# Performance work log

Hardware: AMD Instinct MI355X
Metric: run time of the kernel (lower is better)

The kernel has to match this reference:

```python
import jax, jax.numpy as jnp
import numpy as np

B, N, E, H = 16, 1024, 1024, 16
D = E // H  # head size = 64

def setup_inputs() -> dict:
    key = jax.random.key(0)
    ks = jax.random.split(key, 5)
    s = 1.0 / np.sqrt(E)
    return {
        "x": jax.random.normal(ks[0], (B, N, E), dtype=jnp.float32),
        "W_qkv": jax.random.normal(ks[1], (E, 3 * E), dtype=jnp.float32) * s,
        "b_qkv": jnp.zeros((3 * E,), dtype=jnp.float32),
        "W_proj": jax.random.normal(ks[2], (E, E), dtype=jnp.float32) * s,
        "b_proj": jnp.zeros((E,), dtype=jnp.float32),
    }

def reference(x, W_qkv, b_qkv, W_proj, b_proj):
    # qkv projection: [B,N,3E]
    qkv = x @ W_qkv + b_qkv
    q, k, v = jnp.split(qkv, 3, axis=-1)
    # b n (h d) -> b h n d
    def split_heads(t):
        return t.reshape(B, N, H, D).transpose(0, 2, 1, 3)
    q, k, v = split_heads(q), split_heads(k), split_heads(v)
    scale = D ** -0.5
    attn = jnp.einsum('bhnd,bhmd->bhnm', q, k) * scale  # [B,H,N,N]
    attn = jax.nn.softmax(attn, axis=-1)
    # dropout p=0 -> identity
    o = jnp.einsum('bhnm,bhmd->bhnd', attn, v)  # [B,H,N,D]
    o = o.transpose(0, 2, 1, 3).reshape(B, N, E)  # b h n d -> b n (h d)
    return o @ W_proj + b_proj
```

## Files before the change

kernel.cpp:

```cpp
#include <hip/hip_runtime.h>
#include <hip/hip_bf16.h>
#include <math.h>

#define BB 16
#define NN 1024
#define EE 1024
#define HH 16
#define DD 64
#define THREE_E 3072
#define M_TOTAL (BB * NN)

typedef __attribute__((ext_vector_type(8))) short bf16x8;
typedef __attribute__((ext_vector_type(4))) short bf16x4;
typedef __attribute__((ext_vector_type(4))) float floatx4;

#define SCALE_Q 0.18033688011112042f

static __device__ __forceinline__ unsigned short f2bf(float f) {
    union { float f; unsigned u; } x; x.f = f;
    unsigned r = x.u + 0x7fffu + ((x.u >> 16) & 1u);
    return (unsigned short)(r >> 16);
}

static __device__ __forceinline__ float fast_exp2(float x) {
#if __has_builtin(__builtin_amdgcn_exp2f)
    return __builtin_amdgcn_exp2f(x);
#else
    float r; __asm__("v_exp_f32 %0, %1" : "=v"(r) : "v"(x)); return r;
#endif
}

static __device__ __forceinline__ bf16x8 pack8v(floatx4 a, floatx4 b) {
    union { bf16x8 v; unsigned u[4]; } r;
    __hip_bfloat162 t;
    t = __float22bfloat162_rn(make_float2(a[0], a[1])); r.u[0] = *(unsigned*)&t;
    t = __float22bfloat162_rn(make_float2(a[2], a[3])); r.u[1] = *(unsigned*)&t;
    t = __float22bfloat162_rn(make_float2(b[0], b[1])); r.u[2] = *(unsigned*)&t;
    t = __float22bfloat162_rn(make_float2(b[2], b[3])); r.u[3] = *(unsigned*)&t;
    return r.v;
}
static __device__ __forceinline__ bf16x8 pack8f(float4 a, float4 b) {
    union { bf16x8 v; unsigned u[4]; } r;
    __hip_bfloat162 t;
    t = __float22bfloat162_rn(make_float2(a.x, a.y)); r.u[0] = *(unsigned*)&t;
    t = __float22bfloat162_rn(make_float2(a.z, a.w)); r.u[1] = *(unsigned*)&t;
    t = __float22bfloat162_rn(make_float2(b.x, b.y)); r.u[2] = *(unsigned*)&t;
    t = __float22bfloat162_rn(make_float2(b.z, b.w)); r.u[3] = *(unsigned*)&t;
    return r.v;
}

#define ASYNC16(gp, lp)                                                \
    __builtin_amdgcn_global_load_lds(                                  \
        (const __attribute__((address_space(1))) void*)(gp),           \
        (__attribute__((address_space(3))) void*)(lp), 16, 0, 0)

#define DRAIN_VMEM() __asm__ __volatile__("s_waitcnt vmcnt(0)" ::: "memory")

__global__ __launch_bounds__(256) void prep_all(
    const float* __restrict__ x, unsigned short* __restrict__ xb,
    const float* __restrict__ Wqkv, unsigned short* __restrict__ Wqt,
    const float* __restrict__ Wproj, unsigned short* __restrict__ Wpt)
{
    __shared__ float tile[32][33];
    const int bid = blockIdx.x;
    const int t = threadIdx.x;

    if (bid < 8192) {
        int i = bid * 256 + t;
        const float4* xp = (const float4*)x;
        float4 a = xp[i * 2], b = xp[i * 2 + 1];
        *(bf16x8*)&xb[i * 8] = pack8f(a, b);
        return;
    }

    const float* w; unsigned short* wt; int R, C, bx, by;
    if (bid < 8192 + 3072) {
        int local = bid - 8192;
        bx = local % 96; by = local / 96;
        w = Wqkv; wt = Wqt; R = EE; C = THREE_E;
    } else {
        int local = bid - 11264;
        bx = local % 32; by = local / 32;
        w = Wproj; wt = Wpt; R = EE; C = EE;
    }
    const int lr = t >> 5, lc = t & 31;
    const int r0 = by * 32, c0 = bx * 32;
    #pragma unroll
    for (int p = 0; p < 4; ++p)
        tile[lr + p * 8][lc] = w[(size_t)(r0 + lr + p * 8) * C + c0 + lc];
    __syncthreads();
    #pragma unroll
    for (int p = 0; p < 4; ++p) {
        int oc = lr + p * 8;
        float v = tile[lc][oc];
        wt[(size_t)(c0 + oc) * R + r0 + lc] = f2bf(v);
    }
}

__global__ __launch_bounds__(256, 2) void gemm_qkv_mfma(
    const unsigned short* __restrict__ xb,
    const unsigned short* __restrict__ wt,
    const float* __restrict__ bias,
    unsigned short* __restrict__ Qo, unsigned short* __restrict__ Ko,
    unsigned short* __restrict__ Vo)
{
    __shared__ __align__(16) unsigned short As[256 * 64];
    __shared__ __align__(16) unsigned short Bs[128 * 64];

    const int t = threadIdx.x;
    const int w = t >> 6, lane = t & 63;
    const int quad = lane >> 4, l15 = lane & 15;
    const int wm = w >> 1, wn = w & 1;
    const int m0 = blockIdx.y * 256;
    const int n0 = blockIdx.x * 128;
    const int srow = lane >> 3;
    const int sch  = lane & 7;
    const int scw  = (sch ^ srow) * 8;
    const int rb   = l15 & 7;

    floatx4 acc[8][4];
    #pragma unroll
    for (int i = 0; i < 8; ++i)
        #pragma unroll
        for (int j = 0; j < 4; ++j) acc[i][j] = (floatx4){0.f, 0.f, 0.f, 0.f};

    const unsigned short* aG = &xb[(size_t)(m0 + w * 8 + srow) * EE + scw];
    const unsigned short* bG = &wt[(size_t)(n0 + w * 8 + srow) * EE + scw];

    for (int kk = 0; kk < EE; kk += 64) {
        #pragma unroll
        for (int p = 0; p < 8; ++p)
            ASYNC16(aG + kk + (size_t)(p * 32) * EE, &As[(w * 8 + p * 32) * 64]);
        #pragma unroll
        for (int p = 0; p < 4; ++p)
            ASYNC16(bG + kk + (size_t)(p * 32) * EE, &Bs[(w * 8 + p * 32) * 64]);
        DRAIN_VMEM();
        __syncthreads();

        #pragma unroll
        for (int s = 0; s < 2; ++s) {
            const int rsw = (((s << 2) | quad) ^ rb) * 8;
            bf16x8 af[8], bf[4];
            #pragma unroll
            for (int j = 0; j < 4; ++j)
                bf[j] = *(const bf16x8*)&Bs[(wn * 64 + j * 16 + l15) * 64 + rsw];
            #pragma unroll
            for (int i = 0; i < 8; ++i)
                af[i] = *(const bf16x8*)&As[(wm * 128 + i * 16 + l15) * 64 + rsw];
            __builtin_amdgcn_s_setprio(1);
            #pragma unroll
            for (int i = 0; i < 8; ++i)
                #pragma unroll
                for (int j = 0; j < 4; ++j)
                    acc[i][j] = __builtin_amdgcn_mfma_f32_16x16x32_bf16(
                        af[i], bf[j], acc[i][j], 0, 0, 0);
            __builtin_amdgcn_s_setprio(0);
        }
        __syncthreads();
    }

    const int mb = m0 + wm * 128;
    const int nb = n0 + wn * 64;
    #pragma unroll
    for (int i = 0; i < 8; ++i) {
        #pragma unroll
        for (int j = 0; j < 4; ++j) {
            int nc = nb + j * 16;
            int which = nc >> 10;
            int e0 = nc & 1023;
            int h  = e0 >> 6;
            int d0 = e0 & 63;
            float bv = bias[nc + l15];
            #pragma unroll
            for (int r = 0; r < 4; ++r) {
                int m = mb + i * 16 + quad * 4 + r;
                int b = m >> 10, n = m & 1023;
                size_t off = ((size_t)(b * HH + h) * NN + n) * DD + d0 + l15;
                float v = acc[i][j][r] + bv;
                if (which == 0)      Qo[off] = f2bf(v * SCALE_Q);
                else if (which == 1) Ko[off] = f2bf(v);
                else                 Vo[off] = f2bf(v);
            }
        }
    }
}

__global__ __launch_bounds__(256) void attn_mfma(
    const unsigned short* __restrict__ Q,
    const unsigned short* __restrict__ K,
    const unsigned short* __restrict__ Vn,
    unsigned short* __restrict__ O)
{
    __shared__ __align__(16) unsigned short Ks[2][64 * 64];
    __shared__ __align__(16) unsigned short Vs[2][64 * 64];

    const int t    = threadIdx.x;
    const int w    = t >> 6;
    const int quad = (t >> 4) & 3;
    const int l15  = t & 15;
    const int i    = blockIdx.x;
    const int bh   = ((i >> 6) << 3) | (i & 7);
    const int qt   = (i >> 3) & 7;

    const unsigned short* Qg = Q  + (size_t)bh * NN * DD;
    const unsigned short* Kg = K  + (size_t)bh * NN * DD;
    const unsigned short* Vg = Vn + (size_t)bh * NN * DD;

    const int q0 = qt * 128 + w * 32;

    bf16x8 qf[2][2];
    #pragma unroll
    for (int a = 0; a < 2; ++a) {
        qf[a][0] = *(const bf16x8*)&Qg[(size_t)(q0 + a * 16 + l15) * DD + quad * 8];
        qf[a][1] = *(const bf16x8*)&Qg[(size_t)(q0 + a * 16 + l15) * DD + 32 + quad * 8];
    }

    bf16x8 onesA;
    #pragma unroll
    for (int z = 0; z < 8; ++z) onesA[z] = (short)0x3F80;

    floatx4 oa[2][4];
    #pragma unroll
    for (int a = 0; a < 2; ++a)
        #pragma unroll
        for (int jd = 0; jd < 4; ++jd) oa[a][jd] = (floatx4){0.f, 0.f, 0.f, 0.f};
    floatx4 ls[2];
    ls[0] = (floatx4){0.f, 0.f, 0.f, 0.f};
    ls[1] = (floatx4){0.f, 0.f, 0.f, 0.f};

    const int srow = t >> 2;
    const int sc   = t & 3;
    const int swz  = srow & 7;
    const int cbase = ((quad ^ (l15 & 7)) << 3);

    const int Bk = ((srow >> 2) & 3) | (((srow >> 5) & 1) << 2);
    const int c0 = (((srow >> 4) & 1) << 2) | (srow & 3);

    bf16x8 krA0, krA1, vrA0, vrA1;
    bf16x8 krB0, krB1, vrB0, vrB1;

#define LOADKV(T, k0, k1, v0, v1) do {                                      \
    const unsigned short* kg_ = &Kg[(size_t)((T) * 64 + srow) * DD + sc * 16];\
    k0 = *(const bf16x8*)&kg_[0];                                           \
    k1 = *(const bf16x8*)&kg_[8];                                           \
    const unsigned short* vg_ = &Vg[(size_t)((T) * 64 + srow) * DD + sc * 16];\
    v0 = *(const bf16x8*)&vg_[0];                                           \
    v1 = *(const bf16x8*)&vg_[8]; } while (0)

#define WRITEKV(S, k0, k1, v0, v1) do {                                     \
    *(bf16x8*)&Ks[S][srow * 64 + (((2 * sc + 0) ^ swz) << 3)] = k0;         \
    *(bf16x8*)&Ks[S][srow * 64 + (((2 * sc + 1) ^ swz) << 3)] = k1;         \
    _Pragma("unroll")                                                       \
    for (int z = 0; z < 8; ++z) {                                           \
        const int swb = ((Bk ^ z) << 3) + c0;                               \
        const int dB = (sc * 16 + z) * 64;                                  \
        Vs[S][dB + swb]       = v0[z];                                      \
        Vs[S][dB + 512 + swb] = v1[z];                                      \
    } } while (0)

#define COMPUTE(S) do {                                                     \
    floatx4 sa[2][4];                                                       \
    _Pragma("unroll")                                                       \
    for (int a = 0; a < 2; ++a)                                             \
        _Pragma("unroll")                                                   \
        for (int tt = 0; tt < 4; ++tt) sa[a][tt] = (floatx4){0.f,0.f,0.f,0.f};\
    __builtin_amdgcn_s_setprio(1);                                          \
    _Pragma("unroll")                                                       \
    for (int tt = 0; tt < 4; ++tt) {                                        \
        const unsigned short* kb = &Ks[S][(tt * 16 + l15) * 64];            \
        bf16x8 kf0 = *(const bf16x8*)&kb[cbase];                            \
        bf16x8 kf1 = *(const bf16x8*)&kb[cbase ^ 32];                       \
        _Pragma("unroll")                                                   \
        for (int a = 0; a < 2; ++a) {                                       \
            sa[a][tt] = __builtin_amdgcn_mfma_f32_16x16x32_bf16(            \
                kf0, qf[a][0], sa[a][tt], 0, 0, 0);                         \
            sa[a][tt] = __builtin_amdgcn_mfma_f32_16x16x32_bf16(            \
                kf1, qf[a][1], sa[a][tt], 0, 0, 0);                         \
        }                                                                   \
    }                                                                       \
    __builtin_amdgcn_s_setprio(0);                                          \
    bf16x8 pf[2][2];                                                        \
    _Pragma("unroll")                                                       \
    for (int a = 0; a < 2; ++a) {                                           \
        floatx4 pe[4];                                                      \
        _Pragma("unroll")                                                   \
        for (int tt = 0; tt < 4; ++tt) {                                    \
            _Pragma("unroll")                                               \
            for (int r = 0; r < 4; ++r)                                     \
                pe[tt][r] = fast_exp2(sa[a][tt][r]);                        \
        }                                                                   \
        pf[a][0] = pack8v(pe[0], pe[1]);                                    \
        pf[a][1] = pack8v(pe[2], pe[3]);                                    \
    }                                                                       \
    __builtin_amdgcn_s_setprio(1);                                          \
    _Pragma("unroll")                                                       \
    for (int a = 0; a < 2; ++a) {                                           \
        ls[a] = __builtin_amdgcn_mfma_f32_16x16x32_bf16(                    \
            onesA, pf[a][0], ls[a], 0, 0, 0);                               \
        ls[a] = __builtin_amdgcn_mfma_f32_16x16x32_bf16(                    \
            onesA, pf[a][1], ls[a], 0, 0, 0);                               \
    }                                                                       \
    _Pragma("unroll")                                                       \
    for (int jd = 0; jd < 4; ++jd) {                                        \
        const unsigned short* vb = &Vs[S][(jd * 16 + l15) * 64];            \
        bf16x8 vf0 = *(const bf16x8*)&vb[cbase];                            \
        bf16x8 vf1 = *(const bf16x8*)&vb[cbase ^ 32];                       \
        _Pragma("unroll")                                                   \
        for (int a = 0; a < 2; ++a) {                                       \
            oa[a][jd] = __builtin_amdgcn_mfma_f32_16x16x32_bf16(            \
                vf0, pf[a][0], oa[a][jd], 0, 0, 0);                         \
            oa[a][jd] = __builtin_amdgcn_mfma_f32_16x16x32_bf16(            \
                vf1, pf[a][1], oa[a][jd], 0, 0, 0);                         \
        }                                                                   \
    }                                                                       \
    __builtin_amdgcn_s_setprio(0); } while (0)

    LOADKV(0, krA0, krA1, vrA0, vrA1);
    WRITEKV(0, krA0, krA1, vrA0, vrA1);
    LOADKV(1, krB0, krB1, vrB0, vrB1);
    __syncthreads();

    #pragma unroll 1
    for (int p = 0; p < 8; ++p) {
        WRITEKV(1, krB0, krB1, vrB0, vrB1);
        if (p < 7) LOADKV(2 * p + 2, krA0, krA1, vrA0, vrA1);
        COMPUTE(0);
        __syncthreads();
        if (p < 7) {
            WRITEKV(0, krA0, krA1, vrA0, vrA1);
            LOADKV(2 * p + 3, krB0, krB1, vrB0, vrB1);
        }
        COMPUTE(1);
        __syncthreads();
    }
#undef LOADKV
#undef WRITEKV
#undef COMPUTE

    const int b = bh >> 4, h = bh & 15;
    #pragma unroll
    for (int a = 0; a < 2; ++a) {
        float inv = 1.f / ls[a][0];
        int n = q0 + a * 16 + l15;
        size_t base = (size_t)(b * NN + n) * EE + h * DD;
        #pragma unroll
        for (int jd = 0; jd < 4; ++jd) {
            bf16x4 v;
            v[0] = (short)f2bf(oa[a][jd][0] * inv);
            v[1] = (short)f2bf(oa[a][jd][1] * inv);
            v[2] = (short)f2bf(oa[a][jd][2] * inv);
            v[3] = (short)f2bf(oa[a][jd][3] * inv);
            *(bf16x4*)&O[base + jd * 16 + quad * 4] = v;
        }
    }
}

__global__ __launch_bounds__(256, 2) void gemm_proj_mfma(
    const unsigned short* __restrict__ Ob,
    const unsigned short* __restrict__ Bp,
    const float* __restrict__ bias, float* __restrict__ out)
{
    __shared__ __align__(16) unsigned short As[256 * 64];
    __shared__ __align__(16) unsigned short Bs[128 * 64];

    const int t = threadIdx.x;
    const int w = t >> 6, lane = t & 63;
    const int quad = lane >> 4, l15 = lane & 15;
    const int wm = w >> 1, wn = w & 1;
    const int m0 = blockIdx.y * 256;
    const int n0 = blockIdx.x * 128;
    const int srow = lane >> 3;
    const int sch  = lane & 7;
    const int scw  = (sch ^ srow) * 8;
    const int rb   = l15 & 7;

    floatx4 acc[8][4];
    #pragma unroll
    for (int i = 0; i < 8; ++i)
        #pragma unroll
        for (int j = 0; j < 4; ++j) acc[i][j] = (floatx4){0.f, 0.f, 0.f, 0.f};

    const unsigned short* aG = &Ob[(size_t)(m0 + w * 8 + srow) * EE + scw];
    const unsigned short* bG = &Bp[(size_t)(n0 + w * 8 + srow) * EE + scw];

    for (int kk = 0; kk < EE; kk += 64) {
        #pragma unroll
        for (int p = 0; p < 8; ++p)
            ASYNC16(aG + kk + (size_t)(p * 32) * EE, &As[(w * 8 + p * 32) * 64]);
        #pragma unroll
        for (int p = 0; p < 4; ++p)
            ASYNC16(bG + kk + (size_t)(p * 32) * EE, &Bs[(w * 8 + p * 32) * 64]);
        DRAIN_VMEM();
        __syncthreads();

        #pragma unroll
        for (int s = 0; s < 2; ++s) {
            const int rsw = (((s << 2) | quad) ^ rb) * 8;
            bf16x8 af[8], bf[4];
            #pragma unroll
            for (int j = 0; j < 4; ++j)
                bf[j] = *(const bf16x8*)&Bs[(wn * 64 + j * 16 + l15) * 64 + rsw];
            #pragma unroll
            for (int i = 0; i < 8; ++i)
                af[i] = *(const bf16x8*)&As[(wm * 128 + i * 16 + l15) * 64 + rsw];
            __builtin_amdgcn_s_setprio(1);
            #pragma unroll
            for (int i = 0; i < 8; ++i)
                #pragma unroll
                for (int j = 0; j < 4; ++j)
                    acc[i][j] = __builtin_amdgcn_mfma_f32_16x16x32_bf16(
                        af[i], bf[j], acc[i][j], 0, 0, 0);
            __builtin_amdgcn_s_setprio(0);
        }
        __syncthreads();
    }

    const int mb = m0 + wm * 128;
    const int nb = n0 + wn * 64;
    #pragma unroll
    for (int i = 0; i < 8; ++i) {
        #pragma unroll
        for (int j = 0; j < 4; ++j) {
            float bv = bias[nb + j * 16 + l15];
            #pragma unroll
            for (int r = 0; r < 4; ++r) {
                int mrow = mb + i * 16 + quad * 4 + r;
                out[(size_t)mrow * EE + nb + j * 16 + l15] = acc[i][j][r] + bv;
            }
        }
    }
}

extern "C" void kernel_launch(void* const* d_in, const int* in_sizes, int n_in,
                              void* d_out, int out_size, void* d_ws, size_t ws_size,
                              hipStream_t stream) {
    const float* x     = (const float*)d_in[0];
    const float* Wqkv  = (const float*)d_in[1];
    const float* bqkv  = (const float*)d_in[2];
    const float* Wproj = (const float*)d_in[3];
    const float* bproj = (const float*)d_in[4];
    float* out = (float*)d_out;

    const size_t BHND = (size_t)BB * HH * NN * DD;
    unsigned short* Q   = (unsigned short*)d_ws;
    unsigned short* K   = Q   + BHND;
    unsigned short* Vn  = K   + BHND;
    unsigned short* Ob  = Vn  + BHND;
    unsigned short* xb  = Ob  + BHND;
    unsigned short* Wqt = xb  + BHND;
    unsigned short* Wpt = Wqt + (size_t)THREE_E * EE;

    dim3 blk(256);
    prep_all<<<dim3(12288), blk, 0, stream>>>(x, xb, Wqkv, Wqt, Wproj, Wpt);

    gemm_qkv_mfma<<<dim3(THREE_E / 128, M_TOTAL / 256), blk, 0, stream>>>(
        xb, Wqt, bqkv, Q, K, Vn);
    attn_mfma<<<dim3(BB * HH * NN / 128), blk, 0, stream>>>(Q, K, Vn, Ob);
    gemm_proj_mfma<<<dim3(EE / 128, M_TOTAL / 256), blk, 0, stream>>>(
        Ob, Wpt, bproj, out);
}
```

Before: 374.8 us.

## Double-buffer LDS tiles with async prefetch in QKV and projection GEMMs

Both GEMM kernels switch from a single 64-wide K tile, loaded and then fully drained each iteration, to two 32-wide K buffers. The next chunk is prefetched with global_load_lds while the current one is consumed, and a partial vmcnt wait replaces the full drain. The LDS footprint stays the same, but the XOR swizzle changes to fit the 4-chunk row width. In exchange, the K loop runs twice as many iterations with two barriers each.

Result: slower. 393.1 us (+4.9%).

```diff
diff --git a/kernel.cpp b/kernel.cpp
--- a/kernel.cpp
+++ b/kernel.cpp
@@ -53,8 +53,6 @@
     __builtin_amdgcn_global_load_lds(                                  \
         (const __attribute__((address_space(1))) void*)(gp),           \
         (__attribute__((address_space(3))) void*)(lp), 16, 0, 0)
-
-#define DRAIN_VMEM() __asm__ __volatile__("s_waitcnt vmcnt(0)" ::: "memory")
 
 __global__ __launch_bounds__(256) void prep_all(
     const float* __restrict__ x, unsigned short* __restrict__ xb,
@@ -104,8 +102,8 @@
     unsigned short* __restrict__ Qo, unsigned short* __restrict__ Ko,
     unsigned short* __restrict__ Vo)
 {
-    __shared__ __align__(16) unsigned short As[256 * 64];
-    __shared__ __align__(16) unsigned short Bs[128 * 64];
+    __shared__ __align__(16) unsigned short As[2][256 * 32];
+    __shared__ __align__(16) unsigned short Bs[2][128 * 32];
 
     const int t = threadIdx.x;
     const int w = t >> 6, lane = t & 63;
@@ -113,10 +111,10 @@
     const int wm = w >> 1, wn = w & 1;
     const int m0 = blockIdx.y * 256;
     const int n0 = blockIdx.x * 128;
-    const int srow = lane >> 3;
-    const int sch  = lane & 7;
-    const int scw  = (sch ^ srow) * 8;
-    const int rb   = l15 & 7;
+    const int srow = lane >> 2;
+    const int sch  = lane & 3;
+    const int scw  = (sch ^ ((srow ^ (srow >> 2)) & 3)) * 8;
+    const int rsw  = ((quad ^ ((l15 ^ (l15 >> 2)) & 3))) * 8;
 
     floatx4 acc[8][4];
     #pragma unroll
@@ -124,40 +122,51 @@
         #pragma unroll
         for (int j = 0; j < 4; ++j) acc[i][j] = (floatx4){0.f, 0.f, 0.f, 0.f};
 
-    const unsigned short* aG = &xb[(size_t)(m0 + w * 8 + srow) * EE + scw];
-    const unsigned short* bG = &wt[(size_t)(n0 + w * 8 + srow) * EE + scw];
-
-    for (int kk = 0; kk < EE; kk += 64) {
-        #pragma unroll
-        for (int p = 0; p < 8; ++p)
-            ASYNC16(aG + kk + (size_t)(p * 32) * EE, &As[(w * 8 + p * 32) * 64]);
-        #pragma unroll
-        for (int p = 0; p < 4; ++p)
-            ASYNC16(bG + kk + (size_t)(p * 32) * EE, &Bs[(w * 8 + p * 32) * 64]);
-        DRAIN_VMEM();
-        __syncthreads();
-
-        #pragma unroll
-        for (int s = 0; s < 2; ++s) {
-            const int rsw = (((s << 2) | quad) ^ rb) * 8;
-            bf16x8 af[8], bf[4];
+    const unsigned short* aG = &xb[(size_t)(m0 + w * 16 + srow) * EE + scw];
+    const unsigned short* bG = &wt[(size_t)(n0 + w * 16 + srow) * EE + scw];
+
+#define STG(c, sl) do {                                                     \
+    _Pragma("unroll")                                                       \
+    for (int p = 0; p < 4; ++p)                                             \
+        ASYNC16(aG + (c) * 32 + (size_t)(p * 64) * EE,                      \
+                &As[sl][(w * 16 + p * 64) * 32]);                           \
+    _Pragma("unroll")                                                       \
+    for (int p = 0; p < 2; ++p)                                             \
+        ASYNC16(bG + (c) * 32 + (size_t)(p * 64) * EE,                      \
+                &Bs[sl][(w * 16 + p * 64) * 32]);                           \
+    } while (0)
+
+    STG(0, 0);
+
+    #pragma unroll 1
+    for (int c = 0; c < 32; ++c) {
+        const int cur = c & 1;
+        if (c + 1 < 32) {
+            STG(c + 1, cur ^ 1);
+            __asm__ __volatile__("s_waitcnt vmcnt(6)" ::: "memory");
+        } else {
+            __asm__ __volatile__("s_waitcnt vmcnt(0)" ::: "memory");
+        }
+        __builtin_amdgcn_s_barrier();
+
+        bf16x8 af[8], bfv[4];
+        #pragma unroll
+        for (int j = 0; j < 4; ++j)
+            bfv[j] = *(const bf16x8*)&Bs[cur][(wn * 64 + j * 16 + l15) * 32 + rsw];
+        #pragma unroll
+        for (int i = 0; i < 8; ++i)
+            af[i] = *(const bf16x8*)&As[cur][(wm * 128 + i * 16 + l15) * 32 + rsw];
+        __builtin_amdgcn_s_setprio(1);
+        #pragma unroll
+        for (int i = 0; i < 8; ++i)
             #pragma unroll
             for (int j = 0; j < 4; ++j)
-                bf[j] = *(const bf16x8*)&Bs[(wn * 64 + j * 16 + l15) * 64 + rsw];
-            #pragma unroll
-            for (int i = 0; i < 8; ++i)
-                af[i] = *(const bf16x8*)&As[(wm * 128 + i * 16 + l15) * 64 + rsw];
-            __builtin_amdgcn_s_setprio(1);
-            #pragma unroll
-            for (int i = 0; i < 8; ++i)
-                #pragma unroll
-                for (int j = 0; j < 4; ++j)
-                    acc[i][j] = __builtin_amdgcn_mfma_f32_16x16x32_bf16(
-                        af[i], bf[j], acc[i][j], 0, 0, 0);
-            __builtin_amdgcn_s_setprio(0);
-        }
-        __syncthreads();
-    }
+                acc[i][j] = __builtin_amdgcn_mfma_f32_16x16x32_bf16(
+                    af[i], bfv[j], acc[i][j], 0, 0, 0);
+        __builtin_amdgcn_s_setprio(0);
+        __builtin_amdgcn_s_barrier();
+    }
+#undef STG
 
     const int mb = m0 + wm * 128;
     const int nb = n0 + wn * 64;
@@ -360,8 +369,8 @@
     const unsigned short* __restrict__ Bp,
     const float* __restrict__ bias, float* __restrict__ out)
 {
-    __shared__ __align__(16) unsigned short As[256 * 64];
-    __shared__ __align__(16) unsigned short Bs[128 * 64];
+    __shared__ __align__(16) unsigned short As[2][256 * 32];
+    __shared__ __align__(16) unsigned short Bs[2][128 * 32];
 
     const int t = threadIdx.x;
     const int w = t >> 6, lane = t & 63;
@@ -369,10 +378,10 @@
     const int wm = w >> 1, wn = w & 1;
     const int m0 = blockIdx.y * 256;
     const int n0 = blockIdx.x * 128;
-    const int srow = lane >> 3;
-    const int sch  = lane & 7;
-    const int scw  = (sch ^ srow) * 8;
-    const int rb   = l15 & 7;
+    const int srow = lane >> 2;
+    const int sch  = lane & 3;
+    const int scw  = (sch ^ ((srow ^ (srow >> 2)) & 3)) * 8;
+    const int rsw  = ((quad ^ ((l15 ^ (l15 >> 2)) & 3))) * 8;
 
     floatx4 acc[8][4];
     #pragma unroll
@@ -380,40 +389,51 @@
         #pragma unroll
         for (int j = 0; j < 4; ++j) acc[i][j] = (floatx4){0.f, 0.f, 0.f, 0.f};
 
-    const unsigned short* aG = &Ob[(size_t)(m0 + w * 8 + srow) * EE + scw];
-    const unsigned short* bG = &Bp[(size_t)(n0 + w * 8 + srow) * EE + scw];
-
-    for (int kk = 0; kk < EE; kk += 64) {
-        #pragma unroll
-        for (int p = 0; p < 8; ++p)
-            ASYNC16(aG + kk + (size_t)(p * 32) * EE, &As[(w * 8 + p * 32) * 64]);
-        #pragma unroll
-        for (int p = 0; p < 4; ++p)
-            ASYNC16(bG + kk + (size_t)(p * 32) * EE, &Bs[(w * 8 + p * 32) * 64]);
-        DRAIN_VMEM();
-        __syncthreads();
-
-        #pragma unroll
-        for (int s = 0; s < 2; ++s) {
-            const int rsw = (((s << 2) | quad) ^ rb) * 8;
-            bf16x8 af[8], bf[4];
+    const unsigned short* aG = &Ob[(size_t)(m0 + w * 16 + srow) * EE + scw];
+    const unsigned short* bG = &Bp[(size_t)(n0 + w * 16 + srow) * EE + scw];
+
+#define STG(c, sl) do {                                                     \
+    _Pragma("unroll")                                                       \
+    for (int p = 0; p < 4; ++p)                                             \
+        ASYNC16(aG + (c) * 32 + (size_t)(p * 64) * EE,                      \
+                &As[sl][(w * 16 + p * 64) * 32]);                           \
+    _Pragma("unroll")                                                       \
+    for (int p = 0; p < 2; ++p)                                             \
+        ASYNC16(bG + (c) * 32 + (size_t)(p * 64) * EE,                      \
+                &Bs[sl][(w * 16 + p * 64) * 32]);                           \
+    } while (0)
+
+    STG(0, 0);
+
+    #pragma unroll 1
+    for (int c = 0; c < 32; ++c) {
+        const int cur = c & 1;
+        if (c + 1 < 32) {
+            STG(c + 1, cur ^ 1);
+            __asm__ __volatile__("s_waitcnt vmcnt(6)" ::: "memory");
+        } else {
+            __asm__ __volatile__("s_waitcnt vmcnt(0)" ::: "memory");
+        }
+        __builtin_amdgcn_s_barrier();
+
+        bf16x8 af[8], bfv[4];
+        #pragma unroll
+        for (int j = 0; j < 4; ++j)
+            bfv[j] = *(const bf16x8*)&Bs[cur][(wn * 64 + j * 16 + l15) * 32 + rsw];
+        #pragma unroll
+        for (int i = 0; i < 8; ++i)
+            af[i] = *(const bf16x8*)&As[cur][(wm * 128 + i * 16 + l15) * 32 + rsw];
+        __builtin_amdgcn_s_setprio(1);
+        #pragma unroll
+        for (int i = 0; i < 8; ++i)
             #pragma unroll
             for (int j = 0; j < 4; ++j)
-                bf[j] = *(const bf16x8*)&Bs[(wn * 64 + j * 16 + l15) * 64 + rsw];
-            #pragma unroll
-            for (int i = 0; i < 8; ++i)
-                af[i] = *(const bf16x8*)&As[(wm * 128 + i * 16 + l15) * 64 + rsw];
-            __builtin_amdgcn_s_setprio(1);
-            #pragma unroll
-            for (int i = 0; i < 8; ++i)
-                #pragma unroll
-                for (int j = 0; j < 4; ++j)
-                    acc[i][j] = __builtin_amdgcn_mfma_f32_16x16x32_bf16(
-                        af[i], bf[j], acc[i][j], 0, 0, 0);
-            __builtin_amdgcn_s_setprio(0);
-        }
-        __syncthreads();
-    }
+                acc[i][j] = __builtin_amdgcn_mfma_f32_16x16x32_bf16(
+                    af[i], bfv[j], acc[i][j], 0, 0, 0);
+        __builtin_amdgcn_s_setprio(0);
+        __builtin_amdgcn_s_barrier();
+    }
+#undef STG
 
     const int mb = m0 + wm * 128;
     const int nb = n0 + wn * 64;
```
